# Kernel tuning notes

Measured on AMD Instinct MI355X. Metric: run time of the kernel, lower is better.

Reference implementation:

```python
import jax, jax.numpy as jnp
import numpy as np


def setup_inputs() -> dict:
    key = jax.random.key(0)
    ks = jax.random.split(key, 12)
    B, T, S, D, A, E, L, V = 32, 64, 64, 1024, 512, 256, 1024, 12000
    s = 0.02  # weight scale for numerical stability
    return {
        "targets": jax.random.randint(ks[0], (B, T), 0, V),
        "options": jax.random.normal(ks[1], (B, S, D), jnp.float32),
        "h0": jax.random.normal(ks[2], (B, L), jnp.float32),
        "c0": jnp.zeros((B, L), jnp.float32),
        "emb": jax.random.normal(ks[3], (V, E), jnp.float32) * s,
        "W1": jax.random.normal(ks[4], (L, A), jnp.float32) * s,
        "b1": jnp.zeros((A,), jnp.float32),
        "W2": jax.random.normal(ks[5], (D, A), jnp.float32) * s,
        "b2": jnp.zeros((A,), jnp.float32),
        "Va": jax.random.normal(ks[6], (A, 1), jnp.float32) * s,
        "bVa": jnp.zeros((1,), jnp.float32),
        "Wx": jax.random.normal(ks[7], (D + E, 4 * L), jnp.float32) * s,
        "Wh": jax.random.normal(ks[8], (L, 4 * L), jnp.float32) * s,
        "bl": jnp.zeros((4 * L,), jnp.float32),
        "Wd": jax.random.normal(ks[9], (L, V), jnp.float32) * s,
        "bd": jnp.zeros((V,), jnp.float32),
    }


def reference(targets, options, h0, c0, emb, W1, b1, W2, b2, Va, bVa,
              Wx, Wh, bl, Wd, bd):
    L = h0.shape[-1]
    # W2(options) is step-invariant: hoist out of recurrent loop. [B,S,A]
    opt_proj = jnp.einsum('bsd,da->bsa', options, W2) + b2

    def step(carry, x_ids):
        h, c = carry
        # Bahdanau attention: score = V(tanh(W1(h) + W2(options)))
        score = jnp.tanh(h @ W1 + b1)[:, None, :] + opt_proj        # [B,S,A]
        score = jnp.einsum('bsa,ao->bso', score, Va) + bVa          # [B,S,1]
        w = jax.nn.softmax(score, axis=1)                           # [B,S,1]
        context = jnp.sum(w * options, axis=1)                      # [B,D]
        x = jnp.concatenate([context, emb[x_ids]], axis=-1)         # [B,D+E]
        # Keras LSTM cell, gate order i, f, g, o
        z = x @ Wx + h @ Wh + bl                                    # [B,4L]
        i, f, g, o = jnp.split(z, 4, axis=-1)
        c = jax.nn.sigmoid(f) * c + jax.nn.sigmoid(i) * jnp.tanh(g)
        h = jax.nn.sigmoid(o) * jnp.tanh(c)
        probs = jax.nn.softmax(h @ Wd + bd, axis=-1)                # [B,V]
        return (h, c), (probs, w[..., 0])

    (h, c), (out, attn) = jax.lax.scan(step, (h0, c0), targets.T)
    output = jnp.transpose(out, (1, 0, 2))   # [B,T,V]
    attention = attn[-1][..., None]          # last-step attention weights [B,S,1]
    return output, h, c, attention
```

## Files before the change

### kernel.cpp

```cpp
#include <hip/hip_runtime.h>
#include <math.h>


typedef __bf16 bf16;
typedef _Float16 fp16;
typedef __attribute__((ext_vector_type(8))) __bf16 bf16x8;
typedef __attribute__((ext_vector_type(8))) _Float16 fp16x8;
typedef __attribute__((ext_vector_type(4))) _Float16 fp16x4;
typedef __attribute__((ext_vector_type(4))) float f32x4;

constexpr int B = 32, T = 64, S = 64, D = 1024, A = 512, E = 256, L = 1024, V = 12000;
constexpr int G = 4096;
constexpr size_t N_PROBS = (size_t)B * T * V;

__device__ inline void load_lds16(const void* g, void* l) {
  __builtin_amdgcn_global_load_lds(
      (const __attribute__((address_space(1))) unsigned int*)g,
      (__attribute__((address_space(3))) unsigned int*)l, 16, 0, 0);
}


__global__ void k_v2(const float* __restrict__ W2, const float* __restrict__ Va,
                     float* __restrict__ v2) {
  int gw = (blockIdx.x * blockDim.x + threadIdx.x) >> 6;
  int lane = threadIdx.x & 63;
  if (gw >= D) return;
  float acc = 0.f;
  for (int a = lane; a < A; a += 64) acc += W2[(size_t)gw * A + a] * Va[a];
  #pragma unroll
  for (int off = 32; off; off >>= 1) acc += __shfl_down(acc, off);
  if (lane == 0) v2[gw] = acc;
}

__global__ void k_score(const float* __restrict__ options, const float* __restrict__ v2,
                        float* __restrict__ w) {
  int row = (blockIdx.x * blockDim.x + threadIdx.x) >> 6;
  int lane = threadIdx.x & 63;
  if (row >= B * S) return;
  const float* orow = options + (size_t)row * D;
  float acc = 0.f;
  for (int d = lane; d < D; d += 64) acc += orow[d] * v2[d];
  #pragma unroll
  for (int off = 32; off; off >>= 1) acc += __shfl_down(acc, off);
  if (lane == 0) w[row] = acc;
}

__global__ __launch_bounds__(256) void k_attnctx(
    const float* __restrict__ options, const float* __restrict__ wat,
    float* __restrict__ oattn, float* __restrict__ ctx) {
  __shared__ float sw[64];
  const int b = blockIdx.x, tid = threadIdx.x;
  if (tid < 64) {
    float v = wat[b * 64 + tid];
    float m = v;
    #pragma unroll
    for (int off = 32; off; off >>= 1) m = fmaxf(m, __shfl_xor(m, off));
    float e = expf(v - m);
    float s = e;
    #pragma unroll
    for (int off = 32; off; off >>= 1) s += __shfl_xor(s, off);
    float res = e / s;
    sw[tid] = res;
    oattn[b * 64 + tid] = res;
  }
  __syncthreads();
  for (int d = tid; d < D; d += 256) {
    float acc = 0.f;
    #pragma unroll 8
    for (int s = 0; s < 64; ++s)
      acc += sw[s] * options[((size_t)(b * 64 + s)) * D + d];
    ctx[b * D + d] = acc;
  }
}

__global__ __launch_bounds__(256) void k_cx_part(
    const float* __restrict__ ctx, const float* __restrict__ Wx,
    float* __restrict__ cxp) {
  const int jt = blockIdx.x & 15;
  const int bg = (blockIdx.x >> 4) & 3;
  const int kc = blockIdx.x >> 6;
  const int j = jt * 256 + threadIdx.x;
  const int b0 = bg * 8, d0 = kc * 128;
  float acc[8];
  #pragma unroll
  for (int bb = 0; bb < 8; ++bb) acc[bb] = 0.f;
  for (int d = 0; d < 128; ++d) {
    float wv = Wx[(size_t)(d0 + d) * G + j];
    #pragma unroll
    for (int bb = 0; bb < 8; ++bb)
      acc[bb] = fmaf(ctx[(b0 + bb) * D + d0 + d], wv, acc[bb]);
  }
  #pragma unroll
  for (int bb = 0; bb < 8; ++bb)
    cxp[((size_t)kc * 32 + b0 + bb) * G + j] = acc[bb];
}

__global__ void k_cx_reduce(const float* __restrict__ cxp, const float* __restrict__ bl,
                            float* __restrict__ cx) {
  int i = blockIdx.x * 256 + threadIdx.x;
  float s = bl[i & 4095];
  #pragma unroll
  for (int kc = 0; kc < 8; ++kc) s += cxp[(size_t)kc * 131072 + i];
  cx[i] = s;
}


__global__ void k_eg(const int* __restrict__ targets, const float* __restrict__ emb,
                     fp16* __restrict__ eg) {
  int r = blockIdx.x, e = threadIdx.x;
  int tok = targets[r];
  eg[(size_t)r * E + e] = (fp16)emb[(size_t)tok * E + e];
}

__global__ __launch_bounds__(256) void k_wx2t(const float* __restrict__ Wx,
                                              fp16* __restrict__ t16) {
  __shared__ float s[64][65];
  const int et = blockIdx.x >> 6, jt = blockIdx.x & 63;
  const int e0 = et * 64, j0 = jt * 64;
  const int tid = threadIdx.x;
  const int jj = tid & 63;
  #pragma unroll
  for (int k = 0; k < 16; ++k) {
    int ee = k * 4 + (tid >> 6);
    s[ee][jj] = Wx[(size_t)(D + e0 + ee) * G + j0 + jj];
  }
  __syncthreads();
  const int jc = tid >> 2, eq = tid & 3;
  fp16x8 o0, o1;
  #pragma unroll
  for (int i = 0; i < 8; ++i) {
    o0[i] = (fp16)s[eq * 16 + i][jc];
    o1[i] = (fp16)s[eq * 16 + 8 + i][jc];
  }
  size_t dst = (size_t)(j0 + jc) * E + e0 + eq * 16;
  *(fp16x8*)(t16 + dst) = o0;
  *(fp16x8*)(t16 + dst + 8) = o1;
}

__global__ __launch_bounds__(256) void k_whp(const float* __restrict__ Wh,
                                             fp16* __restrict__ p) {
  __shared__ float s[64][65];
  const int lt = blockIdx.x & 15, ct = blockIdx.x >> 4;
  const int l0 = lt * 64, c0 = ct * 64;
  const int tid = threadIdx.x;
  const int cc = tid & 63;
  #pragma unroll
  for (int k = 0; k < 16; ++k) {
    int ll = k * 4 + (tid >> 6);
    s[ll][cc] = Wh[(size_t)(l0 + ll) * G + c0 + cc];
  }
  __syncthreads();
  const int c = tid >> 2, lq = tid & 3;
  const int col = c0 + c, g = col >> 10, jj = col & 1023;
  const int rowp = ((jj >> 2) << 4) + (g << 2) + (jj & 3);
  fp16x8 o0, o1;
  #pragma unroll
  for (int i = 0; i < 8; ++i) {
    o0[i] = (fp16)s[lq * 16 + i][c];
    o1[i] = (fp16)s[lq * 16 + 8 + i][c];
  }
  size_t dst = (size_t)rowp * L + l0 + lq * 16;
  *(fp16x8*)(p + dst) = o0;
  *(fp16x8*)(p + dst + 8) = o1;
}

__global__ void k_h0split(const float* __restrict__ h0, const float* __restrict__ c0,
                          fp16* __restrict__ h16, float* __restrict__ cst,
                          float* __restrict__ hf32) {
  int i = blockIdx.x * 256 + threadIdx.x;
  float x = h0[i];
  h16[i] = (fp16)x;
  hf32[i] = x;
  cst[i] = c0[i];
}

__global__ __launch_bounds__(256) void k_pre_mfma(
    const fp16* __restrict__ Ag, const fp16* __restrict__ Bg,
    const float* __restrict__ cx, fp16* __restrict__ prep) {
  __shared__ __align__(16) char lds[32768];
  char* sA = lds;
  char* sB = lds + 16384;
  const int bid = blockIdx.x;
  const int swz = (bid & 7) * 64 + (bid >> 3);
  const int mt = swz >> 5, nt = swz & 31;
  const int m0 = mt * 128, n0 = nt * 128;
  const int tid = threadIdx.x, w = tid >> 6, lane = tid & 63;
  const int wr = w >> 1, wc = w & 1;

  f32x4 acc[4][4];
  #pragma unroll
  for (int i = 0; i < 4; ++i)
    #pragma unroll
    for (int j = 0; j < 4; ++j) acc[i][j] = (f32x4){0.f, 0.f, 0.f, 0.f};

  int rowc[4], sloc[4];
  #pragma unroll
  for (int i = 0; i < 4; ++i) {
    int c = i * 4 + w;
    rowc[i] = c * 8 + (lane >> 3);
    sloc[i] = (lane & 7) ^ (rowc[i] & 7);
  }

  for (int kk = 0; kk < 4; ++kk) {
    if (kk) __syncthreads();
    const char* ga = (const char*)Ag + kk * 128;
    const char* gb = (const char*)Bg + kk * 128;
    #pragma unroll
    for (int i = 0; i < 4; ++i) {
      int c = i * 4 + w;
      load_lds16(ga + (size_t)(m0 + rowc[i]) * 512 + sloc[i] * 16, sA + c * 1024);
      load_lds16(gb + (size_t)(n0 + rowc[i]) * 512 + sloc[i] * 16, sB + c * 1024);
    }
    __syncthreads();
    #pragma unroll
    for (int ks = 0; ks < 2; ++ks) {
      fp16x8 av[4], bv[4];
      #pragma unroll
      for (int f = 0; f < 4; ++f) {
        int ra = wr * 64 + f * 16 + (lane & 15);
        int ca = (ks * 4 + (lane >> 4)) ^ (ra & 7);
        av[f] = *(const fp16x8*)(sA + ra * 128 + ca * 16);
        int rb = wc * 64 + f * 16 + (lane & 15);
        int cb = (ks * 4 + (lane >> 4)) ^ (rb & 7);
        bv[f] = *(const fp16x8*)(sB + rb * 128 + cb * 16);
      }
      #pragma unroll
      for (int fm = 0; fm < 4; ++fm)
        #pragma unroll
        for (int fn = 0; fn < 4; ++fn)
          acc[fm][fn] = __builtin_amdgcn_mfma_f32_16x16x32_f16(
              av[fm], bv[fn], acc[fm][fn], 0, 0, 0);
    }
  }

  const int r0o = m0 + wr * 64 + ((lane >> 4) << 2);
  const int c0o = n0 + wc * 64 + (lane & 15);
  #pragma unroll
  for (int fn = 0; fn < 4; ++fn) {
    int colg = c0o + fn * 16;
    int g = colg >> 10, jj = colg & 1023;
    int jb = jj >> 2, jo = jj & 3;
    #pragma unroll
    for (int fm = 0; fm < 4; ++fm) {
      #pragma unroll
      for (int r = 0; r < 4; ++r) {
        int row = r0o + fm * 16 + r;
        int b = row >> 6, t = row & 63;
        float v = acc[fm][fn][r] + cx[(size_t)b * G + colg];
        prep[(((size_t)t * 256 + jb) * 32 + b) * 16 + jo * 4 + g] = (fp16)v;
      }
    }
  }
}

__global__ __launch_bounds__(512) void k_step4(
    const fp16* __restrict__ Whp, const fp16* __restrict__ prep,
    const fp16* __restrict__ hin, fp16* __restrict__ hout,
    float* __restrict__ cst, float* __restrict__ hf32,
    fp16* __restrict__ Hb16, int t) {
  __shared__ float zred[8 * 2 * 64 * 4];
  __shared__ float zf[32][16];
  const int jb = blockIdx.x;
  const int tid = threadIdx.x;
  const int w = tid >> 6, lane = tid & 63;
  const int fr = lane & 15, kc = lane >> 4;

  float pf[4];
  float cprev = 0.f;
  const int gb = tid >> 2, gjo = tid & 3, gj = jb * 4 + gjo;
  if (tid < 128) {
    fp16x4 pv = *(const fp16x4*)(prep + (((size_t)t * 256 + jb) * 32 + gb) * 16 + gjo * 4);
    #pragma unroll
    for (int g = 0; g < 4; ++g) pf[g] = (float)pv[g];
    cprev = cst[gb * 1024 + gj];
  }

  f32x4 acc[2];
  acc[0] = (f32x4){0.f, 0.f, 0.f, 0.f};
  acc[1] = (f32x4){0.f, 0.f, 0.f, 0.f};
  const fp16* bb = Whp + (size_t)(jb * 16 + fr) * L;
  #pragma unroll
  for (int kk = 0; kk < 4; ++kk) {
    const int k0 = (w * 4 + kk) * 32 + kc * 8;
    fp16x8 bv = *(const fp16x8*)(bb + k0);
    #pragma unroll
    for (int m = 0; m < 2; ++m) {
      fp16x8 av = *(const fp16x8*)(hin + (size_t)(m * 16 + fr) * L + k0);
      acc[m] = __builtin_amdgcn_mfma_f32_16x16x32_f16(av, bv, acc[m], 0, 0, 0);
    }
  }
  #pragma unroll
  for (int m = 0; m < 2; ++m)
    *(f32x4*)&zred[((w * 2 + m) * 64 + lane) * 4] = acc[m];
  __syncthreads();
  {
    const int b = tid >> 4, c = tid & 15;
    const int lane2 = (((b & 15) >> 2) << 4) | c;
    const int reg = b & 3, m = b >> 4;
    float s = 0.f;
    #pragma unroll
    for (int ww = 0; ww < 8; ++ww)
      s += zred[((ww * 2 + m) * 64 + lane2) * 4 + reg];
    zf[b][c] = s;
  }
  __syncthreads();
  if (tid < 128) {
    float zi = zf[gb][gjo] + pf[0];
    float zff = zf[gb][4 + gjo] + pf[1];
    float zg = zf[gb][8 + gjo] + pf[2];
    float zo = zf[gb][12 + gjo] + pf[3];
    float si = 1.f / (1.f + expf(-zi));
    float sf = 1.f / (1.f + expf(-zff));
    float tg = tanhf(zg);
    float so = 1.f / (1.f + expf(-zo));
    float cn = sf * cprev + si * tg;
    float hn = so * tanhf(cn);
    const int hi_idx = gb * 1024 + gj;
    cst[hi_idx] = cn;
    hout[hi_idx] = (fp16)hn;
    hf32[hi_idx] = hn;
    Hb16[(size_t)(gb * 64 + t) * L + gj] = (fp16)hn;
  }
}

__global__ __launch_bounds__(256) void k_wdt(const float* __restrict__ Wd,
                                             fp16* __restrict__ Wdt) {
  __shared__ float s[64][65];
  const int lt = blockIdx.x & 15;
  const int vt = blockIdx.x >> 4;
  const int l0 = lt * 64, v0 = vt * 64;
  const int tid = threadIdx.x;
  const int lv = tid & 63;
  #pragma unroll
  for (int k = 0; k < 16; ++k) {
    int ll = k * 4 + (tid >> 6);
    int v = v0 + lv;
    s[ll][lv] = (v < V) ? Wd[(size_t)(l0 + ll) * V + v] : 0.f;
  }
  __syncthreads();
  const int vv = tid >> 2, lq = tid & 3;
  fp16x8 o0, o1;
  #pragma unroll
  for (int j = 0; j < 8; ++j) {
    o0[j] = (fp16)s[lq * 16 + j][vv];
    o1[j] = (fp16)s[lq * 16 + 8 + j][vv];
  }
  fp16* dst = Wdt + (size_t)(v0 + vv) * 1024 + l0 + lq * 16;
  *(fp16x8*)dst = o0;
  *(fp16x8*)(dst + 8) = o1;
}

__global__ __launch_bounds__(256) void k_logits_mfma(
    const fp16* __restrict__ Ag, const fp16* __restrict__ Btg,
    const float* __restrict__ bd, float* __restrict__ out) {
  __shared__ __align__(16) char lds[65536];
  char* sA = lds;
  char* sB = lds + 16384;
  const int bid = blockIdx.x;
  const int wg = (bid & 7) * 188 + (bid >> 3);
  const int nt = wg >> 4, mt = wg & 15;
  const int m0 = mt * 128, n0 = nt * 128;
  const int tid = threadIdx.x, w = tid >> 6, lane = tid & 63;
  const int wr = w >> 1, wc = w & 1;

  f32x4 acc[4][4];
  #pragma unroll
  for (int i = 0; i < 4; ++i)
    #pragma unroll
    for (int j = 0; j < 4; ++j) acc[i][j] = (f32x4){0.f, 0.f, 0.f, 0.f};

  int rowc[4], sloc[4];
  #pragma unroll
  for (int i = 0; i < 4; ++i) {
    int c = i * 4 + w;
    rowc[i] = c * 8 + (lane >> 3);
    sloc[i] = (lane & 7) ^ (rowc[i] & 7);
  }

  for (int kk = 0; kk < 16; ++kk) {
    if (kk) __syncthreads();
    const char* ga = (const char*)Ag + kk * 128;
    const char* gb = (const char*)Btg + kk * 128;
    #pragma unroll
    for (int i = 0; i < 4; ++i) {
      int c = i * 4 + w;
      load_lds16(ga + (size_t)(m0 + rowc[i]) * 2048 + sloc[i] * 16, sA + c * 1024);
      load_lds16(gb + (size_t)(n0 + rowc[i]) * 2048 + sloc[i] * 16, sB + c * 1024);
    }
    __syncthreads();
    #pragma unroll
    for (int ks = 0; ks < 2; ++ks) {
      fp16x8 av[4], bv[4];
      #pragma unroll
      for (int f = 0; f < 4; ++f) {
        int ra = wr * 64 + f * 16 + (lane & 15);
        int ca = (ks * 4 + (lane >> 4)) ^ (ra & 7);
        av[f] = *(const fp16x8*)(sA + ra * 128 + ca * 16);
        int rb = wc * 64 + f * 16 + (lane & 15);
        int cb = (ks * 4 + (lane >> 4)) ^ (rb & 7);
        bv[f] = *(const fp16x8*)(sB + rb * 128 + cb * 16);
      }
      #pragma unroll
      for (int fm = 0; fm < 4; ++fm)
        #pragma unroll
        for (int fn = 0; fn < 4; ++fn)
          acc[fm][fn] = __builtin_amdgcn_mfma_f32_16x16x32_f16(
              av[fm], bv[fn], acc[fm][fn], 0, 0, 0);
    }
  }

  __syncthreads();
  float* ctile = (float*)lds;
  const int c0o = n0 + wc * 64 + (lane & 15);
  #pragma unroll
  for (int fn = 0; fn < 4; ++fn) {
    int colg = c0o + fn * 16;
    float bv = (colg < V) ? bd[colg] : 0.f;
    int col = wc * 64 + fn * 16 + (lane & 15);
    #pragma unroll
    for (int fm = 0; fm < 4; ++fm) {
      int row = wr * 64 + fm * 16 + ((lane >> 4) << 2);
      #pragma unroll
      for (int r = 0; r < 4; ++r)
        ctile[(row + r) * 128 + col] = acc[fm][fn][r] + bv;
    }
  }
  __syncthreads();
  #pragma unroll
  for (int it = 0; it < 16; ++it) {
    int idx = it * 256 + tid;
    int row = idx >> 5, ch = idx & 31;
    int colg = n0 + ch * 4;
    if (colg < V)
      *(float4*)&out[(size_t)(m0 + row) * V + colg] = *(float4*)&ctile[row * 128 + ch * 4];
  }
}

__global__ __launch_bounds__(256) void k_softmax(float* __restrict__ logits) {
  __shared__ float srow[V];
  __shared__ float sred[4];
  float* row = logits + (size_t)blockIdx.x * V;
  const int tid = threadIdx.x;
  const float4* rv = (const float4*)row;
  float4* sv = (float4*)srow;
  float m = -3.4e38f;
  for (int i = tid; i < 3000; i += 256) {
    float4 x = rv[i];
    sv[i] = x;
    m = fmaxf(fmaxf(m, fmaxf(x.x, x.y)), fmaxf(x.z, x.w));
  }
  #pragma unroll
  for (int off = 32; off; off >>= 1) m = fmaxf(m, __shfl_xor(m, off));
  if ((tid & 63) == 0) sred[tid >> 6] = m;
  __syncthreads();
  const float M = fmaxf(fmaxf(sred[0], sred[1]), fmaxf(sred[2], sred[3]));
  float s = 0.f;
  for (int i = tid; i < 3000; i += 256) {
    float4 x = sv[i];
    x.x = __expf(x.x - M); x.y = __expf(x.y - M);
    x.z = __expf(x.z - M); x.w = __expf(x.w - M);
    sv[i] = x;
    s += x.x + x.y + x.z + x.w;
  }
  #pragma unroll
  for (int off = 32; off; off >>= 1) s += __shfl_xor(s, off);
  __syncthreads();
  if ((tid & 63) == 0) sred[tid >> 6] = s;
  __syncthreads();
  const float inv = 1.f / (sred[0] + sred[1] + sred[2] + sred[3]);
  float4* ov = (float4*)row;
  for (int i = tid; i < 3000; i += 256) {
    float4 x = sv[i];
    x.x *= inv; x.y *= inv; x.z *= inv; x.w *= inv;
    ov[i] = x;
  }
}

__global__ void k_finalize(const float* __restrict__ hf32, const float* __restrict__ cst,
                           float* __restrict__ oh, float* __restrict__ oc) {
  int i = blockIdx.x * 256 + threadIdx.x;
  if (i < B * L) {
    oh[i] = hf32[i];
    oc[i] = cst[i];
  }
}


extern "C" void kernel_launch(void* const* d_in, const int* in_sizes, int n_in,
                              void* d_out, int out_size, void* d_ws, size_t ws_size,
                              hipStream_t stream) {
  const int*   targets = (const int*)d_in[0];
  const float* options = (const float*)d_in[1];
  const float* h0      = (const float*)d_in[2];
  const float* c0      = (const float*)d_in[3];
  const float* emb     = (const float*)d_in[4];
  const float* W2      = (const float*)d_in[7];
  const float* Va      = (const float*)d_in[9];
  const float* Wx      = (const float*)d_in[11];
  const float* Wh      = (const float*)d_in[12];
  const float* bl      = (const float*)d_in[13];
  const float* Wd      = (const float*)d_in[14];
  const float* bd      = (const float*)d_in[15];

  float* out      = (float*)d_out;
  float* out_h    = out + N_PROBS;
  float* out_c    = out_h + (size_t)B * L;
  float* out_attn = out_c + (size_t)B * L;

  char* wsb = (char*)d_ws;
  float* v2     = (float*)(wsb);
  float* wat    = (float*)(wsb + 4096);
  float* ctx    = (float*)(wsb + 12288);
  float* cx     = (float*)(wsb + 143360);
  float* cst    = (float*)(wsb + 667648);
  fp16*  hA     = (fp16*)(wsb + 798720);
  fp16*  hB     = (fp16*)(wsb + 864256);
  float* hf32   = (float*)(wsb + 929792);
  fp16*  Eg16   = (fp16*)(wsb + 1191936);
  fp16*  Wx2t16 = (fp16*)(wsb + 2240512);
  fp16*  Hb16   = (fp16*)(wsb + 1191936);
  fp16*  Whp    = (fp16*)(wsb + 7483392);
  fp16*  prep   = (fp16*)(wsb + 15872000);
  float* cxp    = (float*)(wsb + 15872000);
  fp16*  Wdt    = (fp16*)(wsb + 7483392);

  k_v2<<<256, 256, 0, stream>>>(W2, Va, v2);
  k_score<<<512, 256, 0, stream>>>(options, v2, wat);
  k_attnctx<<<32, 256, 0, stream>>>(options, wat, out_attn, ctx);
  k_cx_part<<<512, 256, 0, stream>>>(ctx, Wx, cxp);
  k_cx_reduce<<<512, 256, 0, stream>>>(cxp, bl, cx);

  k_eg<<<2048, 256, 0, stream>>>(targets, emb, Eg16);
  k_wx2t<<<256, 256, 0, stream>>>(Wx, Wx2t16);
  k_whp<<<1024, 256, 0, stream>>>(Wh, Whp);

  k_pre_mfma<<<512, 256, 0, stream>>>(Eg16, Wx2t16, cx, prep);
  k_h0split<<<128, 256, 0, stream>>>(h0, c0, hA, cst, hf32);

  for (int t = 0; t < T; ++t) {
    const fp16* hin = (t & 1) ? hB : hA;
    fp16* hout = (t & 1) ? hA : hB;
    k_step4<<<256, 512, 0, stream>>>(Whp, prep, hin, hout, cst, hf32, Hb16, t);
  }

  k_wdt<<<188 * 16, 256, 0, stream>>>(Wd, Wdt);
  k_logits_mfma<<<1504, 256, 0, stream>>>(Hb16, Wdt, bd, out);
  k_softmax<<<B * T, 256, 0, stream>>>(out);
  k_finalize<<<128, 256, 0, stream>>>(hf32, cst, out_h, out_c);
}
```

Baseline: 560.4 us.

## Restructure LSTM step kernel to split batch across waves, removing LDS reduction

The recurrent step kernel now uses 2 waves per block, each owning 16 batch rows and running the full K=1024 reduction itself, instead of 8 waves splitting K and reducing partials through shared memory. Gate values are regrouped across lanes with xor shuffles rather than LDS, so both __syncthreads barriers go away, and four independent accumulators shorten the MFMA dependency chain. The f32 hidden state is written only at the last step. Each wave now does more serial MFMA work and loads the Wh tile redundantly, and the block drops from 512 to 128 threads, which cuts latency hiding per CU.

```diff
diff --git a/kernel.cpp b/kernel.cpp
--- a/kernel.cpp
+++ b/kernel.cpp
@@ -4,7 +4,6 @@
 
 typedef __bf16 bf16;
 typedef _Float16 fp16;
-typedef __attribute__((ext_vector_type(8))) __bf16 bf16x8;
 typedef __attribute__((ext_vector_type(8))) _Float16 fp16x8;
 typedef __attribute__((ext_vector_type(4))) _Float16 fp16x4;
 typedef __attribute__((ext_vector_type(4))) float f32x4;
@@ -253,73 +252,91 @@
   }
 }
 
-__global__ __launch_bounds__(512) void k_step4(
+__global__ __launch_bounds__(128) void k_step5(
     const fp16* __restrict__ Whp, const fp16* __restrict__ prep,
     const fp16* __restrict__ hin, fp16* __restrict__ hout,
     float* __restrict__ cst, float* __restrict__ hf32,
     fp16* __restrict__ Hb16, int t) {
-  __shared__ float zred[8 * 2 * 64 * 4];
-  __shared__ float zf[32][16];
   const int jb = blockIdx.x;
-  const int tid = threadIdx.x;
-  const int w = tid >> 6, lane = tid & 63;
+  const int w = threadIdx.x >> 6;
+  const int lane = threadIdx.x & 63;
   const int fr = lane & 15, kc = lane >> 4;
-
-  float pf[4];
-  float cprev = 0.f;
-  const int gb = tid >> 2, gjo = tid & 3, gj = jb * 4 + gjo;
-  if (tid < 128) {
-    fp16x4 pv = *(const fp16x4*)(prep + (((size_t)t * 256 + jb) * 32 + gb) * 16 + gjo * 4);
-    #pragma unroll
-    for (int g = 0; g < 4; ++g) pf[g] = (float)pv[g];
-    cprev = cst[gb * 1024 + gj];
-  }
-
-  f32x4 acc[2];
-  acc[0] = (f32x4){0.f, 0.f, 0.f, 0.f};
-  acc[1] = (f32x4){0.f, 0.f, 0.f, 0.f};
-  const fp16* bb = Whp + (size_t)(jb * 16 + fr) * L;
-  #pragma unroll
-  for (int kk = 0; kk < 4; ++kk) {
-    const int k0 = (w * 4 + kk) * 32 + kc * 8;
-    fp16x8 bv = *(const fp16x8*)(bb + k0);
-    #pragma unroll
-    for (int m = 0; m < 2; ++m) {
-      fp16x8 av = *(const fp16x8*)(hin + (size_t)(m * 16 + fr) * L + k0);
-      acc[m] = __builtin_amdgcn_mfma_f32_16x16x32_f16(av, bv, acc[m], 0, 0, 0);
-    }
-  }
-  #pragma unroll
-  for (int m = 0; m < 2; ++m)
-    *(f32x4*)&zred[((w * 2 + m) * 64 + lane) * 4] = acc[m];
-  __syncthreads();
-  {
-    const int b = tid >> 4, c = tid & 15;
-    const int lane2 = (((b & 15) >> 2) << 4) | c;
-    const int reg = b & 3, m = b >> 4;
-    float s = 0.f;
-    #pragma unroll
-    for (int ww = 0; ww < 8; ++ww)
-      s += zred[((ww * 2 + m) * 64 + lane2) * 4 + reg];
-    zf[b][c] = s;
-  }
-  __syncthreads();
-  if (tid < 128) {
-    float zi = zf[gb][gjo] + pf[0];
-    float zff = zf[gb][4 + gjo] + pf[1];
-    float zg = zf[gb][8 + gjo] + pf[2];
-    float zo = zf[gb][12 + gjo] + pf[3];
+  const int g = (lane >> 2) & 3, jo = lane & 3;
+  const int hi = lane >> 4;
+  const int gj = jb * 4 + jo;
+
+  float pf[4][4], cp[4];
+  #pragma unroll
+  for (int r = 0; r < 4; ++r) {
+    int b = w * 16 + hi * 4 + r;
+    fp16x4 pv = *(const fp16x4*)(prep + (((size_t)t * 256 + jb) * 32 + b) * 16 + jo * 4);
+    #pragma unroll
+    for (int gg = 0; gg < 4; ++gg) pf[r][gg] = (float)pv[gg];
+    cp[r] = cst[b * 1024 + gj];
+  }
+
+  f32x4 a0 = (f32x4){0.f,0.f,0.f,0.f}, a1 = a0, a2 = a0, a3 = a0;
+  const fp16* bb = Whp + (size_t)(jb * 16 + fr) * 1024 + kc * 8;
+  const fp16* aa = hin + (size_t)(w * 16 + fr) * 1024 + kc * 8;
+  #pragma unroll
+  for (int kk = 0; kk < 32; kk += 4) {
+    a0 = __builtin_amdgcn_mfma_f32_16x16x32_f16(
+        *(const fp16x8*)(aa + (kk + 0) * 32), *(const fp16x8*)(bb + (kk + 0) * 32), a0, 0, 0, 0);
+    a1 = __builtin_amdgcn_mfma_f32_16x16x32_f16(
+        *(const fp16x8*)(aa + (kk + 1) * 32), *(const fp16x8*)(bb + (kk + 1) * 32), a1, 0, 0, 0);
+    a2 = __builtin_amdgcn_mfma_f32_16x16x32_f16(
+        *(const fp16x8*)(aa + (kk + 2) * 32), *(const fp16x8*)(bb + (kk + 2) * 32), a2, 0, 0, 0);
+    a3 = __builtin_amdgcn_mfma_f32_16x16x32_f16(
+        *(const fp16x8*)(aa + (kk + 3) * 32), *(const fp16x8*)(bb + (kk + 3) * 32), a3, 0, 0, 0);
+  }
+  f32x4 z;
+  #pragma unroll
+  for (int q = 0; q < 4; ++q) z[q] = (a0[q] + a1[q]) + (a2[q] + a3[q]);
+
+  f32x4 zx;
+  #pragma unroll
+  for (int q = 0; q < 4; ++q) zx[q] = __shfl_xor(z[q], 4);
+  f32x4 za, zb;
+  #pragma unroll
+  for (int q = 0; q < 4; ++q) {
+    za[q] = (g & 1) ? zx[q] : z[q];
+    zb[q] = (g & 1) ? z[q] : zx[q];
+  }
+  f32x4 za2, zb2;
+  #pragma unroll
+  for (int q = 0; q < 4; ++q) {
+    za2[q] = __shfl_xor(za[q], 8);
+    zb2[q] = __shfl_xor(zb[q], 8);
+  }
+  f32x4 z0, z1, z2, z3;
+  #pragma unroll
+  for (int q = 0; q < 4; ++q) {
+    bool lo = (g < 2);
+    z0[q] = lo ? za[q] : za2[q];
+    z1[q] = lo ? zb[q] : zb2[q];
+    z2[q] = lo ? za2[q] : za[q];
+    z3[q] = lo ? zb2[q] : zb[q];
+  }
+
+  #pragma unroll
+  for (int r = 0; r < 4; ++r) {
+    float zi = z0[r] + pf[r][0];
+    float zf = z1[r] + pf[r][1];
+    float zg = z2[r] + pf[r][2];
+    float zo = z3[r] + pf[r][3];
     float si = 1.f / (1.f + expf(-zi));
-    float sf = 1.f / (1.f + expf(-zff));
+    float sf = 1.f / (1.f + expf(-zf));
     float tg = tanhf(zg);
     float so = 1.f / (1.f + expf(-zo));
-    float cn = sf * cprev + si * tg;
+    float cn = sf * cp[r] + si * tg;
     float hn = so * tanhf(cn);
-    const int hi_idx = gb * 1024 + gj;
-    cst[hi_idx] = cn;
-    hout[hi_idx] = (fp16)hn;
-    hf32[hi_idx] = hn;
-    Hb16[(size_t)(gb * 64 + t) * L + gj] = (fp16)hn;
+    if (g == 0) {
+      int b = w * 16 + hi * 4 + r;
+      cst[b * 1024 + gj] = cn;
+      hout[b * 1024 + gj] = (fp16)hn;
+      Hb16[(size_t)(b * 64 + t) * 1024 + gj] = (fp16)hn;
+      if (t == T - 1) hf32[b * 1024 + gj] = hn;
+    }
   }
 }
 
@@ -540,7 +557,7 @@
   for (int t = 0; t < T; ++t) {
     const fp16* hin = (t & 1) ? hB : hA;
     fp16* hout = (t & 1) ? hA : hB;
-    k_step4<<<256, 512, 0, stream>>>(Whp, prep, hin, hout, cst, hf32, Hb16, t);
+    k_step5<<<256, 128, 0, stream>>>(Whp, prep, hin, hout, cst, hf32, Hb16, t);
   }
 
   k_wdt<<<188 * 16, 256, 0, stream>>>(Wd, Wdt);
```

After: 669.2 us. +19.4%, slower.

## Split recurrent LSTM step across batch halves and read h from history buffer

Applied to the files above, without the earlier changes.

The per-step LSTM kernel now runs 512 blocks of 256 threads, each handling one gate-column tile for half the batch, instead of 256 blocks of 512 threads covering the full batch. The previous hidden state is read directly from the fp16 history buffer Hb16 with a stride, which removes the ping-pong h buffers and the extra hout/hf32 writes on every step. Gate activations use fast __expf-based sigmoid/tanh, and the gates are gathered across lanes with warp shuffles instead of a second LDS pass and barrier. The intent is to shorten each latency-bound recurrent launch, at the cost of strided A-operand loads and slightly less accurate activations.

```diff
diff --git a/kernel.cpp b/kernel.cpp
--- a/kernel.cpp
+++ b/kernel.cpp
@@ -4,7 +4,6 @@
 
 typedef __bf16 bf16;
 typedef _Float16 fp16;
-typedef __attribute__((ext_vector_type(8))) __bf16 bf16x8;
 typedef __attribute__((ext_vector_type(8))) _Float16 fp16x8;
 typedef __attribute__((ext_vector_type(4))) _Float16 fp16x4;
 typedef __attribute__((ext_vector_type(4))) float f32x4;
@@ -253,73 +252,63 @@
   }
 }
 
-__global__ __launch_bounds__(512) void k_step4(
+__global__ __launch_bounds__(256) void k_step6(
     const fp16* __restrict__ Whp, const fp16* __restrict__ prep,
-    const fp16* __restrict__ hin, fp16* __restrict__ hout,
+    const fp16* __restrict__ Aprev, int Ars,
     float* __restrict__ cst, float* __restrict__ hf32,
     fp16* __restrict__ Hb16, int t) {
-  __shared__ float zred[8 * 2 * 64 * 4];
-  __shared__ float zf[32][16];
-  const int jb = blockIdx.x;
+  __shared__ f32x4 zred[4][64];
+  const int jb = blockIdx.x >> 1, bh = blockIdx.x & 1;
   const int tid = threadIdx.x;
   const int w = tid >> 6, lane = tid & 63;
   const int fr = lane & 15, kc = lane >> 4;
 
-  float pf[4];
-  float cprev = 0.f;
-  const int gb = tid >> 2, gjo = tid & 3, gj = jb * 4 + gjo;
-  if (tid < 128) {
-    fp16x4 pv = *(const fp16x4*)(prep + (((size_t)t * 256 + jb) * 32 + gb) * 16 + gjo * 4);
-    #pragma unroll
-    for (int g = 0; g < 4; ++g) pf[g] = (float)pv[g];
-    cprev = cst[gb * 1024 + gj];
-  }
-
-  f32x4 acc[2];
-  acc[0] = (f32x4){0.f, 0.f, 0.f, 0.f};
-  acc[1] = (f32x4){0.f, 0.f, 0.f, 0.f};
-  const fp16* bb = Whp + (size_t)(jb * 16 + fr) * L;
-  #pragma unroll
-  for (int kk = 0; kk < 4; ++kk) {
-    const int k0 = (w * 4 + kk) * 32 + kc * 8;
-    fp16x8 bv = *(const fp16x8*)(bb + k0);
-    #pragma unroll
-    for (int m = 0; m < 2; ++m) {
-      fp16x8 av = *(const fp16x8*)(hin + (size_t)(m * 16 + fr) * L + k0);
-      acc[m] = __builtin_amdgcn_mfma_f32_16x16x32_f16(av, bv, acc[m], 0, 0, 0);
-    }
-  }
-  #pragma unroll
-  for (int m = 0; m < 2; ++m)
-    *(f32x4*)&zred[((w * 2 + m) * 64 + lane) * 4] = acc[m];
-  __syncthreads();
-  {
-    const int b = tid >> 4, c = tid & 15;
-    const int lane2 = (((b & 15) >> 2) << 4) | c;
-    const int reg = b & 3, m = b >> 4;
-    float s = 0.f;
-    #pragma unroll
-    for (int ww = 0; ww < 8; ++ww)
-      s += zred[((ww * 2 + m) * 64 + lane2) * 4 + reg];
-    zf[b][c] = s;
-  }
-  __syncthreads();
-  if (tid < 128) {
-    float zi = zf[gb][gjo] + pf[0];
-    float zff = zf[gb][4 + gjo] + pf[1];
-    float zg = zf[gb][8 + gjo] + pf[2];
-    float zo = zf[gb][12 + gjo] + pf[3];
-    float si = 1.f / (1.f + expf(-zi));
-    float sf = 1.f / (1.f + expf(-zff));
-    float tg = tanhf(zg);
-    float so = 1.f / (1.f + expf(-zo));
-    float cn = sf * cprev + si * tg;
-    float hn = so * tanhf(cn);
-    const int hi_idx = gb * 1024 + gj;
-    cst[hi_idx] = cn;
-    hout[hi_idx] = (fp16)hn;
-    hf32[hi_idx] = hn;
-    Hb16[(size_t)(gb * 64 + t) * L + gj] = (fp16)hn;
+  f32x4 a0 = (f32x4){0.f, 0.f, 0.f, 0.f}, a1 = a0;
+  const fp16* bb = Whp + (size_t)(jb * 16 + fr) * 1024 + w * 256 + kc * 8;
+  const fp16* aa = Aprev + (size_t)(bh * 16 + fr) * Ars + w * 256 + kc * 8;
+  #pragma unroll
+  for (int kk = 0; kk < 8; kk += 2) {
+    a0 = __builtin_amdgcn_mfma_f32_16x16x32_f16(
+        *(const fp16x8*)(aa + kk * 32), *(const fp16x8*)(bb + kk * 32), a0, 0, 0, 0);
+    a1 = __builtin_amdgcn_mfma_f32_16x16x32_f16(
+        *(const fp16x8*)(aa + (kk + 1) * 32), *(const fp16x8*)(bb + (kk + 1) * 32), a1, 0, 0, 0);
+  }
+  f32x4 zv;
+  #pragma unroll
+  for (int q = 0; q < 4; ++q) zv[q] = a0[q] + a1[q];
+  zred[w][lane] = zv;
+  __syncthreads();
+
+  const int b_local = tid >> 4, col = tid & 15;
+  const int b = bh * 16 + b_local;
+  const int g = col >> 2, jo = col & 3;
+  const int lane2 = ((b_local >> 2) << 4) | col;
+  const int reg = b_local & 3;
+  float z = zred[0][lane2][reg] + zred[1][lane2][reg]
+          + zred[2][lane2][reg] + zred[3][lane2][reg];
+  z += (float)prep[(((size_t)t * 256 + jb) * 32 + b) * 16 + jo * 4 + g];
+  float act;
+  if (g == 2) act = 1.f - 2.f / (1.f + __expf(2.f * z));
+  else        act = 1.f / (1.f + __expf(-z));
+  float x4 = __shfl_xor(act, 4);
+  float za = (g & 1) ? x4 : act;
+  float zb = (g & 1) ? act : x4;
+  float za2 = __shfl_xor(za, 8);
+  float zb2 = __shfl_xor(zb, 8);
+  const bool lo = (g < 2);
+  float Ai = lo ? za : za2;
+  float Af = lo ? zb : zb2;
+  float Ag_ = lo ? za2 : za;
+  float Ao = lo ? zb2 : zb;
+  if (g == 0) {
+    const int gj = jb * 4 + jo;
+    float cp = cst[b * 1024 + gj];
+    float cn = Af * cp + Ai * Ag_;
+    float th = 1.f - 2.f / (1.f + __expf(2.f * cn));
+    float hn = Ao * th;
+    cst[b * 1024 + gj] = cn;
+    Hb16[((size_t)b * 64 + t) * 1024 + gj] = (fp16)hn;
+    if (t == T - 1) hf32[b * 1024 + gj] = hn;
   }
 }
 
@@ -514,7 +503,6 @@
   float* cx     = (float*)(wsb + 143360);
   float* cst    = (float*)(wsb + 667648);
   fp16*  hA     = (fp16*)(wsb + 798720);
-  fp16*  hB     = (fp16*)(wsb + 864256);
   float* hf32   = (float*)(wsb + 929792);
   fp16*  Eg16   = (fp16*)(wsb + 1191936);
   fp16*  Wx2t16 = (fp16*)(wsb + 2240512);
@@ -538,9 +526,9 @@
   k_h0split<<<128, 256, 0, stream>>>(h0, c0, hA, cst, hf32);
 
   for (int t = 0; t < T; ++t) {
-    const fp16* hin = (t & 1) ? hB : hA;
-    fp16* hout = (t & 1) ? hA : hB;
-    k_step4<<<256, 512, 0, stream>>>(Whp, prep, hin, hout, cst, hf32, Hb16, t);
+    const fp16* Aprev = (t == 0) ? hA : (Hb16 + (size_t)(t - 1) * 1024);
+    int Ars = (t == 0) ? 1024 : 65536;
+    k_step6<<<512, 256, 0, stream>>>(Whp, prep, Aprev, Ars, cst, hf32, Hb16, t);
   }
 
   k_wdt<<<188 * 16, 256, 0, stream>>>(Wd, Wdt);
```

Result: slower. 607.5 us (+8.4%).
